# Optimization experiments

Hardware: AMD Instinct MI355X
Metric: run time of the kernel (lower is better)

## Reference

```python
import jax, jax.numpy as jnp
import numpy as np

LAMBDA = 0.5
TAU = 1.0
EPS = 1e-8  # torch F.cosine_similarity eps

B, D = 8192, 1024


def setup_inputs() -> dict:
    key = jax.random.key(0)
    k1, k2, k3, k4 = jax.random.split(key, 4)
    return {
        "student_query_emb": jax.random.normal(k1, (B, D), dtype=jnp.float32),
        "student_passage_emb": jax.random.normal(k2, (B, D), dtype=jnp.float32),
        "teacher_query_emb": jax.random.normal(k3, (B, D), dtype=jnp.float32),
        "teacher_passage_emb": jax.random.normal(k4, (B, D), dtype=jnp.float32),
    }


def _mse(a, b):
    d = a - b
    return jnp.mean(d * d)


def _retrieval_loss(q, p):
    # cosine sim = (q . p) / max(||q|| * ||p||, eps); normalize then matmul
    # (avoids the [B,B,D] broadcast intermediate of the torch version)
    qn = q / jnp.maximum(jnp.linalg.norm(q, axis=-1, keepdims=True), EPS)
    pn = p / jnp.maximum(jnp.linalg.norm(p, axis=-1, keepdims=True), EPS)
    logits = jnp.einsum("bd,cd->bc", qn, pn) / TAU  # [B, B]
    # cross-entropy with labels = arange(B): pick the diagonal log-prob
    logprobs = jax.nn.log_softmax(logits, axis=-1)
    return -jnp.mean(jnp.diagonal(logprobs))


def reference(student_query_emb, student_passage_emb, teacher_query_emb, teacher_passage_emb):
    distill = 0.5 * (_mse(student_query_emb, teacher_query_emb)
                     + _mse(student_passage_emb, teacher_passage_emb))
    retrieval = _retrieval_loss(student_query_emb, student_passage_emb)
    return LAMBDA * distill + (1.0 - LAMBDA) * retrieval
```

## Files before the change

kernel.cpp:

```cpp
#include <hip/hip_runtime.h>
#include <hip/hip_bf16.h>

typedef unsigned short u16;
typedef unsigned char u8;
typedef float f32x4 __attribute__((ext_vector_type(4)));
typedef int int4v __attribute__((ext_vector_type(4)));
typedef int int8v __attribute__((ext_vector_type(8)));

#define B_ROWS 8192
#define D_DIM  1024
#define FP8_SCALE 16.0f
#define ACC_UNSCALE (1.0f/256.0f)


__global__ void __launch_bounds__(256) prep_kernel(
    const float* __restrict__ sq, const float* __restrict__ sp,
    const float* __restrict__ tq, const float* __restrict__ tp,
    int* __restrict__ qn, int* __restrict__ pn,
    float* __restrict__ ppq, float* __restrict__ ppp, float* __restrict__ ppd)
{
    const int wave = threadIdx.x >> 6;
    const int l    = threadIdx.x & 63;
    const int r    = blockIdx.x * 4 + wave;
    const size_t rb4 = (size_t)r * (D_DIM / 4);

    const float4* Q4 = (const float4*)sq + rb4;
    const float4* P4 = (const float4*)sp + rb4;
    const float4* A4 = (const float4*)tq + rb4;
    const float4* B4 = (const float4*)tp + rb4;

    float4 qv[4], pv[4];
    float sq2 = 0.f, sp2 = 0.f, dq = 0.f, dp = 0.f, qp = 0.f;
    #pragma unroll
    for (int j = 0; j < 4; ++j) {
        const int idx = j * 64 + l;
        float4 q = Q4[idx], p = P4[idx], a = A4[idx], b = B4[idx];
        qv[j] = q; pv[j] = p;
        sq2 += q.x*q.x + q.y*q.y + q.z*q.z + q.w*q.w;
        sp2 += p.x*p.x + p.y*p.y + p.z*p.z + p.w*p.w;
        float dx = q.x-a.x, dy = q.y-a.y, dz = q.z-a.z, dw = q.w-a.w;
        dq += dx*dx + dy*dy + dz*dz + dw*dw;
        dx = p.x-b.x; dy = p.y-b.y; dz = p.z-b.z; dw = p.w-b.w;
        dp += dx*dx + dy*dy + dz*dz + dw*dw;
        qp += q.x*p.x + q.y*p.y + q.z*p.z + q.w*p.w;
    }

    #pragma unroll
    for (int m = 1; m <= 32; m <<= 1) {
        sq2 += __shfl_xor(sq2, m);
        sp2 += __shfl_xor(sp2, m);
        dq  += __shfl_xor(dq, m);
        dp  += __shfl_xor(dp, m);
        qp  += __shfl_xor(qp, m);
    }

    const float rq = 1.0f / fmaxf(sqrtf(sq2), 1e-8f);
    const float rp = 1.0f / fmaxf(sqrtf(sp2), 1e-8f);

    if (l == 0) {
        ppq[r] = dq;
        ppp[r] = dp;
        ppd[r] = qp * rq * rp;
    }

    const float fq = rq * FP8_SCALE;
    const float fp = rp * FP8_SCALE;
    int* qrow = qn + (size_t)r * (D_DIM / 4);
    int* prow = pn + (size_t)r * (D_DIM / 4);
    #pragma unroll
    for (int j = 0; j < 4; ++j) {
        const int idx = j * 64 + l;
        int pk = __builtin_amdgcn_cvt_pk_fp8_f32(qv[j].x * fq, qv[j].y * fq, 0, false);
        pk     = __builtin_amdgcn_cvt_pk_fp8_f32(qv[j].z * fq, qv[j].w * fq, pk, true);
        qrow[idx] = pk;
        pk = __builtin_amdgcn_cvt_pk_fp8_f32(pv[j].x * fp, pv[j].y * fp, 0, false);
        pk = __builtin_amdgcn_cvt_pk_fp8_f32(pv[j].z * fp, pv[j].w * fp, pk, true);
        prow[idx] = pk;
    }
}

__global__ void __launch_bounds__(256) gemm_rowsum_kernel(
    const u8* __restrict__ Q, const u8* __restrict__ P,
    float* __restrict__ gpart)
{
    __shared__ u8 smA[128 * 128];
    __shared__ u8 smB[128 * 128];

    const int tid  = threadIdx.x;
    const int wave = tid >> 6;
    const int lane = tid & 63;
    const int bm = blockIdx.y;
    const int bn = blockIdx.x;

    const int lrow   = lane >> 3;
    const int gchunk = (lane & 7) ^ lrow;
    const u8* Ag = Q + ((size_t)bm * 128) * D_DIM + gchunk * 16;
    const u8* Bg = P + ((size_t)bn * 128) * D_DIM + gchunk * 16;

    const int quad  = lane >> 4;
    const int rw    = lane & 15;
    const int r7    = lane & 7;
    const int arow0 = (wave >> 1) * 64;
    const int bcol0 = (wave & 1) * 64;

    const int off_lo = ((2 * quad) ^ r7) * 16;
    const int off_hi = ((2 * quad + 1) ^ r7) * 16;

    f32x4 acc[4][4];
    #pragma unroll
    for (int i = 0; i < 4; ++i)
        #pragma unroll
        for (int j = 0; j < 4; ++j)
            acc[i][j] = (f32x4){0.f, 0.f, 0.f, 0.f};

    for (int k0 = 0; k0 < D_DIM; k0 += 128) {
        #pragma unroll
        for (int i = 0; i < 4; ++i) {
            const int r0 = wave * 32 + i * 8;
            __builtin_amdgcn_global_load_lds(
                (const __attribute__((address_space(1))) void*)(Ag + (size_t)(r0 + lrow) * D_DIM + k0),
                (__attribute__((address_space(3))) void*)(smA + r0 * 128), 16, 0, 0);
            __builtin_amdgcn_global_load_lds(
                (const __attribute__((address_space(1))) void*)(Bg + (size_t)(r0 + lrow) * D_DIM + k0),
                (__attribute__((address_space(3))) void*)(smB + r0 * 128), 16, 0, 0);
        }
        __syncthreads();

        union Frag { int8v v8; struct { int4v lo, hi; } h; };
        Frag af[4], bf[4];
        #pragma unroll
        for (int mi = 0; mi < 4; ++mi)
            af[mi].h.lo = *(const int4v*)(smA + (arow0 + mi * 16 + rw) * 128 + off_lo);
        #pragma unroll
        for (int ni = 0; ni < 4; ++ni)
            bf[ni].h.lo = *(const int4v*)(smB + (bcol0 + ni * 16 + rw) * 128 + off_lo);
        __builtin_amdgcn_sched_barrier(0);
        #pragma unroll
        for (int mi = 0; mi < 4; ++mi)
            af[mi].h.hi = *(const int4v*)(smA + (arow0 + mi * 16 + rw) * 128 + off_hi);
        #pragma unroll
        for (int ni = 0; ni < 4; ++ni)
            bf[ni].h.hi = *(const int4v*)(smB + (bcol0 + ni * 16 + rw) * 128 + off_hi);

        #pragma unroll
        for (int mi = 0; mi < 4; ++mi)
            #pragma unroll
            for (int ni = 0; ni < 4; ++ni)
                acc[mi][ni] = __builtin_amdgcn_mfma_scale_f32_16x16x128_f8f6f4(
                    af[mi].v8, bf[ni].v8, acc[mi][ni],
                    0, 0,
                    0, 0x7f7f7f7f,
                    0, 0x7f7f7f7f);
        __syncthreads();
    }

    float esum[4][4];
    #pragma unroll
    for (int mi = 0; mi < 4; ++mi)
        #pragma unroll
        for (int r = 0; r < 4; ++r) {
            float s = 0.f;
            #pragma unroll
            for (int ni = 0; ni < 4; ++ni)
                s += __expf(acc[mi][ni][r] * ACC_UNSCALE);
            esum[mi][r] = s;
        }
    #pragma unroll
    for (int m = 1; m <= 8; m <<= 1)
        #pragma unroll
        for (int mi = 0; mi < 4; ++mi)
            #pragma unroll
            for (int r = 0; r < 4; ++r)
                esum[mi][r] += __shfl_xor(esum[mi][r], m);

    if (rw == 0) {
        float* dst = gpart + ((size_t)(bn * 2 + (wave & 1))) * B_ROWS
                   + bm * 128 + arow0;
        #pragma unroll
        for (int mi = 0; mi < 4; ++mi)
            #pragma unroll
            for (int r = 0; r < 4; ++r)
                dst[mi * 16 + quad * 4 + r] = esum[mi][r];
    }
}

__global__ void __launch_bounds__(256) reduce_kernel(
    const float* __restrict__ gpart,
    const float* __restrict__ ppq, const float* __restrict__ ppp,
    const float* __restrict__ ppd, float4* __restrict__ bpart)
{
    const int t = threadIdx.x;
    const int r = blockIdx.x * 256 + t;
    float s = 0.f;
    #pragma unroll 8
    for (int j = 0; j < 128; ++j) s += gpart[(size_t)j * B_ROWS + r];
    float ls = logf(s);
    float v2 = ppq[r], v3 = ppp[r], v4 = ppd[r];
    #pragma unroll
    for (int m = 1; m <= 32; m <<= 1) {
        ls += __shfl_xor(ls, m);
        v2 += __shfl_xor(v2, m);
        v3 += __shfl_xor(v3, m);
        v4 += __shfl_xor(v4, m);
    }
    __shared__ float red[4][4];
    if ((t & 63) == 0) {
        red[t >> 6][0] = ls; red[t >> 6][1] = v2;
        red[t >> 6][2] = v3; red[t >> 6][3] = v4;
    }
    __syncthreads();
    if (t == 0) {
        float4 o;
        o.x = red[0][0] + red[1][0] + red[2][0] + red[3][0];
        o.y = red[0][1] + red[1][1] + red[2][1] + red[3][1];
        o.z = red[0][2] + red[1][2] + red[2][2] + red[3][2];
        o.w = red[0][3] + red[1][3] + red[2][3] + red[3][3];
        bpart[blockIdx.x] = o;
    }
}

__global__ void __launch_bounds__(64) finalize_kernel(
    const float4* __restrict__ bpart, float* __restrict__ out)
{
    const int t = threadIdx.x;
    float4 v = (t < 32) ? bpart[t] : (float4){0.f, 0.f, 0.f, 0.f};
    #pragma unroll
    for (int m = 1; m <= 16; m <<= 1) {
        v.x += __shfl_xor(v.x, m);
        v.y += __shfl_xor(v.y, m);
        v.z += __shfl_xor(v.z, m);
        v.w += __shfl_xor(v.w, m);
    }
    if (t == 0) {
        const float inv_bd = 1.0f / ((float)B_ROWS * (float)D_DIM);
        float distill   = 0.5f * (v.y + v.z) * inv_bd;
        float retrieval = (v.x - v.w) / (float)B_ROWS;
        out[0] = 0.5f * distill + 0.5f * retrieval;
    }
}

extern "C" void kernel_launch(void* const* d_in, const int* in_sizes, int n_in,
                              void* d_out, int out_size, void* d_ws, size_t ws_size,
                              hipStream_t stream) {
    const float* sq = (const float*)d_in[0];
    const float* sp = (const float*)d_in[1];
    const float* tq = (const float*)d_in[2];
    const float* tp = (const float*)d_in[3];

    char* ws = (char*)d_ws;
    float*  ppq   = (float*)(ws);
    float*  ppp   = (float*)(ws + 32768);
    float*  ppd   = (float*)(ws + 65536);
    float4* bpart = (float4*)(ws + 98304);
    float*  gpart = (float*)(ws + 131072);
    int*    qn    = (int*)(ws + 131072 + (size_t)128 * B_ROWS * 4);
    int*    pn    = (int*)((char*)qn + (size_t)B_ROWS * D_DIM);

    prep_kernel<<<B_ROWS / 4, 256, 0, stream>>>(sq, sp, tq, tp, qn, pn, ppq, ppp, ppd);
    gemm_rowsum_kernel<<<dim3(64, 64), 256, 0, stream>>>((const u8*)qn, (const u8*)pn, gpart);
    reduce_kernel<<<32, 256, 0, stream>>>(gpart, ppq, ppp, ppd, bpart);
    finalize_kernel<<<1, 64, 0, stream>>>(bpart, (float*)d_out);
}
```

Baseline: 242.4 us.

## Use 256x256 tiles with double-buffered LDS and interleaved async prefetch

The FP8 GEMM+rowsum kernel moves from 128x128 tiles with 4 waves to 256x256 tiles with 8 waves. LDS is double-buffered, and the global-to-LDS loads for the next k-steps are interleaved between MFMA groups, with explicit vmcnt waits and raised instruction priority around the MFMAs. The aim is to overlap memory with compute and halve global traffic per FLOP. In exchange it uses 128KB of LDS, more accumulator registers (32 f32x4), and a fully unrolled k loop. Output partials are still 128 columns per row, since 32 column-blocks times 4 waves equals the old 64 times 2.

```diff
diff --git a/kernel.cpp b/kernel.cpp
--- a/kernel.cpp
+++ b/kernel.cpp
@@ -79,84 +79,122 @@
     }
 }
 
-__global__ void __launch_bounds__(256) gemm_rowsum_kernel(
+union Frag { int8v v8; struct { int4v lo, hi; } h; };
+
+__global__ void __launch_bounds__(512, 2) gemm_rowsum_kernel(
     const u8* __restrict__ Q, const u8* __restrict__ P,
     float* __restrict__ gpart)
 {
-    __shared__ u8 smA[128 * 128];
-    __shared__ u8 smB[128 * 128];
+    __shared__ u8 smA[2][256 * 128];
+    __shared__ u8 smB[2][256 * 128];
 
     const int tid  = threadIdx.x;
     const int wave = tid >> 6;
     const int lane = tid & 63;
-    const int bm = blockIdx.y;
-    const int bn = blockIdx.x;
-
-    const int lrow   = lane >> 3;
-    const int gchunk = (lane & 7) ^ lrow;
-    const u8* Ag = Q + ((size_t)bm * 128) * D_DIM + gchunk * 16;
-    const u8* Bg = P + ((size_t)bn * 128) * D_DIM + gchunk * 16;
-
-    const int quad  = lane >> 4;
-    const int rw    = lane & 15;
-    const int r7    = lane & 7;
-    const int arow0 = (wave >> 1) * 64;
-    const int bcol0 = (wave & 1) * 64;
-
+    const int wm   = wave >> 2;
+    const int wn   = wave & 3;
+    const int bm   = blockIdx.y;
+    const int bn   = blockIdx.x;
+
+    const int srow   = tid >> 3;
+    const int schunk = (tid & 7) ^ (srow & 7);
+    const u8* Ag = Q + (size_t)(bm * 256 + srow) * D_DIM + schunk * 16;
+    const u8* Bg = P + (size_t)(bn * 256 + srow) * D_DIM + schunk * 16;
+    const int ldsw = wave * 1024;
+
+#define STAGE_A(b, rbase, k0)                                                  \
+    __builtin_amdgcn_global_load_lds(                                          \
+        (const __attribute__((address_space(1))) void*)(Ag + (size_t)(rbase) * D_DIM + (k0)), \
+        (__attribute__((address_space(3))) void*)(&smA[b][(rbase) * 128] + ldsw), 16, 0, 0)
+#define STAGE_B(b, rbase, k0)                                                  \
+    __builtin_amdgcn_global_load_lds(                                          \
+        (const __attribute__((address_space(1))) void*)(Bg + (size_t)(rbase) * D_DIM + (k0)), \
+        (__attribute__((address_space(3))) void*)(&smB[b][(rbase) * 128] + ldsw), 16, 0, 0)
+
+    const int quad = lane >> 4;
+    const int rw   = lane & 15;
+    const int r7   = lane & 7;
     const int off_lo = ((2 * quad) ^ r7) * 16;
     const int off_hi = ((2 * quad + 1) ^ r7) * 16;
-
-    f32x4 acc[4][4];
-    #pragma unroll
-    for (int i = 0; i < 4; ++i)
+    const int arow_base = (wm * 128 + rw) * 128;
+    const int brow_base = (wn * 64  + rw) * 128;
+
+    f32x4 acc[8][4];
+    #pragma unroll
+    for (int i = 0; i < 8; ++i)
         #pragma unroll
         for (int j = 0; j < 4; ++j)
             acc[i][j] = (f32x4){0.f, 0.f, 0.f, 0.f};
 
-    for (int k0 = 0; k0 < D_DIM; k0 += 128) {
-        #pragma unroll
-        for (int i = 0; i < 4; ++i) {
-            const int r0 = wave * 32 + i * 8;
-            __builtin_amdgcn_global_load_lds(
-                (const __attribute__((address_space(1))) void*)(Ag + (size_t)(r0 + lrow) * D_DIM + k0),
-                (__attribute__((address_space(3))) void*)(smA + r0 * 128), 16, 0, 0);
-            __builtin_amdgcn_global_load_lds(
-                (const __attribute__((address_space(1))) void*)(Bg + (size_t)(r0 + lrow) * D_DIM + k0),
-                (__attribute__((address_space(3))) void*)(smB + r0 * 128), 16, 0, 0);
-        }
-        __syncthreads();
-
-        union Frag { int8v v8; struct { int4v lo, hi; } h; };
-        Frag af[4], bf[4];
-        #pragma unroll
-        for (int mi = 0; mi < 4; ++mi)
-            af[mi].h.lo = *(const int4v*)(smA + (arow0 + mi * 16 + rw) * 128 + off_lo);
-        #pragma unroll
-        for (int ni = 0; ni < 4; ++ni)
-            bf[ni].h.lo = *(const int4v*)(smB + (bcol0 + ni * 16 + rw) * 128 + off_lo);
-        __builtin_amdgcn_sched_barrier(0);
-        #pragma unroll
-        for (int mi = 0; mi < 4; ++mi)
-            af[mi].h.hi = *(const int4v*)(smA + (arow0 + mi * 16 + rw) * 128 + off_hi);
-        #pragma unroll
-        for (int ni = 0; ni < 4; ++ni)
-            bf[ni].h.hi = *(const int4v*)(smB + (bcol0 + ni * 16 + rw) * 128 + off_hi);
-
-        #pragma unroll
-        for (int mi = 0; mi < 4; ++mi)
-            #pragma unroll
-            for (int ni = 0; ni < 4; ++ni)
-                acc[mi][ni] = __builtin_amdgcn_mfma_scale_f32_16x16x128_f8f6f4(
-                    af[mi].v8, bf[ni].v8, acc[mi][ni],
-                    0, 0,
-                    0, 0x7f7f7f7f,
-                    0, 0x7f7f7f7f);
-        __syncthreads();
-    }
-
-    float esum[4][4];
-    #pragma unroll
-    for (int mi = 0; mi < 4; ++mi)
+    STAGE_A(0, 0, 0);   STAGE_A(0, 64, 0);   STAGE_A(0, 128, 0);   STAGE_A(0, 192, 0);
+    STAGE_B(0, 0, 0);   STAGE_B(0, 64, 0);   STAGE_B(0, 128, 0);   STAGE_B(0, 192, 0);
+    STAGE_A(1, 0, 128); STAGE_A(1, 64, 128); STAGE_A(1, 128, 128); STAGE_A(1, 192, 128);
+    STAGE_B(1, 0, 128); STAGE_B(1, 64, 128);
+
+#define MFMA_QUAD(mih, nih)                                                    \
+    _Pragma("unroll")                                                          \
+    for (int mi = 0; mi < 4; ++mi)                                             \
+      _Pragma("unroll")                                                        \
+      for (int ni = 0; ni < 2; ++ni)                                           \
+        acc[(mih)*4 + mi][(nih)*2 + ni] =                                      \
+            __builtin_amdgcn_mfma_scale_f32_16x16x128_f8f6f4(                  \
+                af[(mih)*4 + mi].v8, bf[(nih)*2 + ni].v8,                      \
+                acc[(mih)*4 + mi][(nih)*2 + ni],                               \
+                0, 0, 0, 0x7f7f7f7f, 0, 0x7f7f7f7f);
+
+#define KSTEP(t, DO_B1, DO_T2, VMN)                                            \
+  {                                                                            \
+    constexpr int cur = (t) & 1;                                               \
+    if (DO_B1) { STAGE_B(cur ^ 1, 128, ((t) + 1) * 128);                       \
+                 STAGE_B(cur ^ 1, 192, ((t) + 1) * 128); }                     \
+    asm volatile("s_waitcnt vmcnt(" #VMN ")" ::: "memory");                    \
+    __builtin_amdgcn_s_barrier();                                              \
+    __builtin_amdgcn_sched_barrier(0);                                         \
+    Frag af[8], bf[4];                                                         \
+    const u8* sA_ = &smA[cur][0];                                              \
+    const u8* sB_ = &smB[cur][0];                                              \
+    _Pragma("unroll")                                                          \
+    for (int mi = 0; mi < 8; ++mi)                                             \
+      af[mi].h.lo = *(const int4v*)(sA_ + arow_base + mi * 2048 + off_lo);     \
+    _Pragma("unroll")                                                          \
+    for (int ni = 0; ni < 4; ++ni)                                             \
+      bf[ni].h.lo = *(const int4v*)(sB_ + brow_base + ni * 2048 + off_lo);     \
+    __builtin_amdgcn_sched_barrier(0);                                         \
+    _Pragma("unroll")                                                          \
+    for (int mi = 0; mi < 8; ++mi)                                             \
+      af[mi].h.hi = *(const int4v*)(sA_ + arow_base + mi * 2048 + off_hi);     \
+    _Pragma("unroll")                                                          \
+    for (int ni = 0; ni < 4; ++ni)                                             \
+      bf[ni].h.hi = *(const int4v*)(sB_ + brow_base + ni * 2048 + off_hi);     \
+    asm volatile("s_waitcnt lgkmcnt(0)" ::: "memory");                         \
+    __builtin_amdgcn_sched_barrier(0);                                         \
+    __builtin_amdgcn_s_barrier();                                              \
+    __builtin_amdgcn_s_setprio(1); MFMA_QUAD(0, 0) __builtin_amdgcn_s_setprio(0); \
+    if (DO_T2) { STAGE_A(cur, 0,   ((t) + 2) * 128); STAGE_A(cur, 64,  ((t) + 2) * 128); } \
+    __builtin_amdgcn_s_setprio(1); MFMA_QUAD(0, 1) __builtin_amdgcn_s_setprio(0); \
+    if (DO_T2) { STAGE_A(cur, 128, ((t) + 2) * 128); STAGE_A(cur, 192, ((t) + 2) * 128); } \
+    __builtin_amdgcn_s_setprio(1); MFMA_QUAD(1, 0) __builtin_amdgcn_s_setprio(0); \
+    if (DO_T2) { STAGE_B(cur, 0,   ((t) + 2) * 128); STAGE_B(cur, 64,  ((t) + 2) * 128); } \
+    __builtin_amdgcn_s_setprio(1); MFMA_QUAD(1, 1) __builtin_amdgcn_s_setprio(0); \
+  }
+
+    KSTEP(0, true,  true,  8)
+    KSTEP(1, true,  true,  8)
+    KSTEP(2, true,  true,  8)
+    KSTEP(3, true,  true,  8)
+    KSTEP(4, true,  true,  8)
+    KSTEP(5, true,  true,  8)
+    KSTEP(6, true,  false, 8)
+    KSTEP(7, false, false, 0)
+
+#undef KSTEP
+#undef MFMA_QUAD
+#undef STAGE_A
+#undef STAGE_B
+
+    float esum[8][4];
+    #pragma unroll
+    for (int mi = 0; mi < 8; ++mi)
         #pragma unroll
         for (int r = 0; r < 4; ++r) {
             float s = 0.f;
@@ -168,16 +206,16 @@
     #pragma unroll
     for (int m = 1; m <= 8; m <<= 1)
         #pragma unroll
-        for (int mi = 0; mi < 4; ++mi)
+        for (int mi = 0; mi < 8; ++mi)
             #pragma unroll
             for (int r = 0; r < 4; ++r)
                 esum[mi][r] += __shfl_xor(esum[mi][r], m);
 
     if (rw == 0) {
-        float* dst = gpart + ((size_t)(bn * 2 + (wave & 1))) * B_ROWS
-                   + bm * 128 + arow0;
+        float* dst = gpart + (size_t)(bn * 4 + wn) * B_ROWS
+                   + bm * 256 + wm * 128;
         #pragma unroll
-        for (int mi = 0; mi < 4; ++mi)
+        for (int mi = 0; mi < 8; ++mi)
             #pragma unroll
             for (int r = 0; r < 4; ++r)
                 dst[mi * 16 + quad * 4 + r] = esum[mi][r];
@@ -257,7 +295,7 @@
     int*    pn    = (int*)((char*)qn + (size_t)B_ROWS * D_DIM);
 
     prep_kernel<<<B_ROWS / 4, 256, 0, stream>>>(sq, sp, tq, tp, qn, pn, ppq, ppp, ppd);
-    gemm_rowsum_kernel<<<dim3(64, 64), 256, 0, stream>>>((const u8*)qn, (const u8*)pn, gpart);
+    gemm_rowsum_kernel<<<dim3(32, 32), 512, 0, stream>>>((const u8*)qn, (const u8*)pn, gpart);
     reduce_kernel<<<32, 256, 0, stream>>>(gpart, ppq, ppp, ppd, bpart);
     finalize_kernel<<<1, 64, 0, stream>>>(bpart, (float*)d_out);
 }
```

New measurement: 234.2 us. 1.03x faster.
